# Optimization experiments

Measured on AMD Instinct MI355X. Metric: run time of the kernel, lower is better.

Reference implementation:

```python
import jax, jax.numpy as jnp
import numpy as np

# ---- static config (matches init_kwargs) ----
B, N, DIM = 1, 2048, 1024
H, KVH, D = 16, 8, 64
GQ = H // KVH                 # grouped queries per kv head
WS = 64                       # sliding window size (causal, exact)
CBS, STRIDE = 32, 16          # compress block size / sliding stride
SEL_BLK, NSEL, NMEM = 32, 4, 1
NCB = N // STRIDE             # num compressed blocks (128)
NFB = N // SEL_BLK            # num fine blocks (64)
NCPF = SEL_BLK // STRIDE      # compressed blocks per fine block (2)
HID = CBS * D                 # compress MLP hidden (expand factor 1.0)
SCALE = D ** -0.5
THETA = 10000.0
NEG = -jnp.finfo(jnp.float32).max


def setup_inputs():
    key = jax.random.key(0)
    ks = jax.random.split(key, 16)
    s = 0.02
    r = lambda i, shape: jax.random.normal(ks[i], shape, jnp.float32) * s
    return {
        "inp": jax.random.normal(ks[0], (B, N, DIM), jnp.float32),
        "norm_g": jnp.ones((DIM,), jnp.float32),
        "Wqkv": r(1, (DIM, (H + 2 * KVH) * D)),
        "mem_kv": r(2, (2, KVH, NMEM, D)),
        "k_pos": r(3, (KVH, CBS, D)),
        "v_pos": r(4, (KVH, CBS, D)),
        "kW1": r(5, (CBS * D, HID)), "kb1": jnp.zeros((HID,), jnp.float32),
        "kW2": r(6, (HID, D)), "kb2": jnp.zeros((D,), jnp.float32),
        "vW1": r(7, (CBS * D, HID)), "vb1": jnp.zeros((HID,), jnp.float32),
        "vW2": r(8, (HID, D)), "vb2": jnp.zeros((D,), jnp.float32),
        "combW": r(9, (DIM, 3 * H)),
        "combB": jnp.tile(jnp.array([-2.0, -2.0, 2.0], jnp.float32), H),
        "Wout": r(10, (H * D, DIM)),
    }


def _rope(t):
    # lucidrains rotary-embedding-torch: interleaved adjacent-pair rotation
    inv_freq = 1.0 / (THETA ** (jnp.arange(0, D, 2, dtype=jnp.float32) / D))
    ang = jnp.arange(N, dtype=jnp.float32)[:, None] * inv_freq        # [N, D/2]
    cos = jnp.repeat(jnp.cos(ang), 2, axis=-1)                        # [N, D]
    sin = jnp.repeat(jnp.sin(ang), 2, axis=-1)
    t2 = t.reshape(*t.shape[:-1], D // 2, 2)
    rot = jnp.stack([-t2[..., 1], t2[..., 0]], axis=-1).reshape(t.shape)
    return t * cos + rot * sin


def _forward(inp, norm_g, Wqkv, mem_kv, k_pos, v_pos,
             kW1, kb1, kW2, kb2, vW1, vb1, vW2, vb2,
             combW, combB, Wout):
    # RMSNorm
    x = inp * jax.lax.rsqrt(jnp.mean(inp * inp, -1, keepdims=True)
                            + jnp.finfo(inp.dtype).eps) * norm_g
    qkv = x @ Wqkv
    q, k, v = jnp.split(qkv, [H * D, H * D + KVH * D], axis=-1)
    q = q.reshape(B, N, H, D).transpose(0, 2, 1, 3)      # b h n d
    k = k.reshape(B, N, KVH, D).transpose(0, 2, 1, 3)    # b kvh n d
    v = v.reshape(B, N, KVH, D).transpose(0, 2, 1, 3)

    # ---- compressed branch (overlapping windows, left zero pad) ----
    overlap = CBS - STRIDE
    kp = jnp.pad(k, ((0, 0), (0, 0), (overlap, 0), (0, 0)))
    vp = jnp.pad(v, ((0, 0), (0, 0), (overlap, 0), (0, 0)))
    widx = jnp.arange(NCB)[:, None] * STRIDE + jnp.arange(CBS)[None, :]  # [NCB, CBS]
    kw = kp[:, :, widx] + k_pos[None, :, None]   # b kvh w cbs d
    vw = vp[:, :, widx] + v_pos[None, :, None]

    def cmlp(t, W1, b1, W2, b2):
        t = t.reshape(B, KVH, NCB, CBS * D)
        return jax.nn.relu(t @ W1 + b1) @ W2 + b2       # b kvh w d

    ck = cmlp(kw, kW1, kb1, kW2, kb2)
    cv = cmlp(vw, vW1, vb1, vW2, vb2)
    ck = jnp.concatenate([jnp.broadcast_to(mem_kv[0], (B, KVH, NMEM, D)), ck], 2)
    cv = jnp.concatenate([jnp.broadcast_to(mem_kv[1], (B, KVH, NMEM, D)), cv], 2)

    qg = q.reshape(B, KVH, GQ, N, D)
    csim = jnp.einsum('bhgid,bhjd->bhgij', qg, ck) * SCALE   # no mask (cmask=None)
    cattn = jax.nn.softmax(csim, -1)
    cout = jnp.einsum('bhgij,bhjd->bhgid', cattn, cv).reshape(B, H, N, D)

    # rotary AFTER compressed attention (as in source)
    rq, rk = _rope(q), _rope(k)

    # ---- importance scores -> top-k fine block selection ----
    imp = csim[..., NMEM:].mean(2)                          # b kvh n NCB (share grouped q)
    imp = imp.reshape(B, KVH, N, NFB, NCPF).mean(-1)        # mean-pool to fine blocks
    q_blk = jnp.arange(N) // SEL_BLK
    diag = q_blk[:, None] == jnp.arange(NFB)[None, :]
    imp = jnp.where(diag[None, None], NEG, imp)             # mask own (diagonal) block
    imp = jax.nn.softmax(jnp.pad(imp, ((0, 0),) * 3 + ((1, 0),),
                                 constant_values=-1000.0), -1)[..., 1:]
    sel_val, sel_idx = jax.lax.top_k(imp, NSEL)             # b kvh n NSEL

    # ---- fine (block-selected) attention ----
    own = jnp.broadcast_to(q_blk[None, None, :, None], (B, KVH, N, 1))
    sel_idx = jnp.concatenate([sel_idx, own], -1)           # append own block
    fmask = jnp.repeat((sel_val > 1e-10)[..., None], SEL_BLK, -1)  # b kvh n NSEL blk
    causal_row = jnp.tril(jnp.ones((SEL_BLK, SEL_BLK), bool))[jnp.arange(N) % SEL_BLK]
    causal = jnp.broadcast_to(causal_row[None, None, :, None, :],
                              (B, KVH, N, 1, SEL_BLK))
    fmask = jnp.concatenate([fmask, causal], 3).reshape(B, KVH, N, (NSEL + 1) * SEL_BLK)

    fk_blocks = rk.reshape(B, KVH, NFB, SEL_BLK, D)
    fv_blocks = v.reshape(B, KVH, NFB, SEL_BLK, D)
    gather = jax.vmap(jax.vmap(lambda blocks, idx: blocks[idx]))  # over b, kvh
    fk = gather(fk_blocks, sel_idx).reshape(B, KVH, N, (NSEL + 1) * SEL_BLK, D)
    fv = gather(fv_blocks, sel_idx).reshape(B, KVH, N, (NSEL + 1) * SEL_BLK, D)

    rqg = rq.reshape(B, KVH, GQ, N, D)
    fsim = jnp.einsum('bhgid,bhijd->bhgij', rqg, fk) * SCALE
    fsim = jnp.where(fmask[:, :, None], fsim, NEG / 10)
    fattn = jax.nn.softmax(fsim, -1)
    fout = jnp.einsum('bhgij,bhijd->bhgid', fattn, fv).reshape(B, H, N, D)

    # ---- sliding window (causal, exact window size WS) ----
    NW = N // WS
    kp2 = jnp.pad(rk, ((0, 0), (0, 0), (WS, 0), (0, 0)))
    vp2 = jnp.pad(v, ((0, 0), (0, 0), (WS, 0), (0, 0)))
    kidx = jnp.arange(NW)[:, None] * WS + jnp.arange(2 * WS)[None, :]
    kwin = kp2[:, :, kidx]                                  # b kvh nw 2ws d
    vwin = vp2[:, :, kidx]
    qwin = rqg.reshape(B, KVH, GQ, NW, WS, D)
    ssim = jnp.einsum('bhgwid,bhwjd->bhgwij', qwin, kwin) * SCALE
    i = jnp.arange(WS)[:, None]
    j = jnp.arange(2 * WS)[None, :]
    diff = i - (j - WS)
    local_ok = (diff >= 0) & (diff < WS)                    # [WS, 2WS]
    keypos = jnp.arange(NW)[:, None, None] * WS + (jnp.arange(2 * WS) - WS)[None, None, :]
    smask = local_ok[None] & (keypos >= 0)                  # [NW, WS, 2WS]
    ssim = jnp.where(smask[None, None, None], ssim, NEG)
    sattn = jax.nn.softmax(ssim, -1)
    sout = jnp.einsum('bhgwij,bhwjd->bhgwid', sattn, vwin).reshape(B, H, N, D)

    # ---- learned strategy combination (compressed, fine, sliding) ----
    gates = jax.nn.sigmoid(x @ combW + combB).reshape(B, N, H, 3).transpose(0, 2, 1, 3)
    out = gates[..., 0:1] * cout + gates[..., 1:2] * fout + gates[..., 2:3] * sout
    out = out.transpose(0, 2, 1, 3).reshape(B, N, H * D) @ Wout
    return out


def reference(inp, norm_g, Wqkv, mem_kv, k_pos, v_pos,
              kW1, kb1, kW2, kb2, vW1, vb1, vW2, vb2,
              combW, combB, Wout):
    return _forward(inp, norm_g, Wqkv, mem_kv, k_pos, v_pos,
                    kW1, kb1, kW2, kb2, vW1, vb1, vW2, vb2,
                    combW, combB, Wout)
```

## Files before the change

kernel.cpp:

```cpp
#include <hip/hip_runtime.h>
#include <hip/hip_bf16.h>

#define NTOK 2048
#define DIM 1024
#define NH 16
#define KVH 8
#define GQ 2
#define HD 64
#define WS 64
#define CBS 32
#define STRIDE 16
#define SEL_BLK 32
#define NSEL 4
#define NMEM 1
#define NCB 128
#define NFB 64
#define HIDN 2048
#define SCALE 0.125f
#define NEGF (-3.4028234663852886e38f)
#define NEG10F (-3.4028234663852886e37f)

typedef __attribute__((ext_vector_type(8))) short bf16x8;
typedef __attribute__((ext_vector_type(4))) float f32x4;

__device__ __forceinline__ float bflo(unsigned u) { return __uint_as_float(u << 16); }
__device__ __forceinline__ float bfhi(unsigned u) { return __uint_as_float(u & 0xffff0000u); }
__device__ __forceinline__ void dot8(const float4& qa, const float4& qb, uint4 a, float& s) {
    s += qa.x * bflo(a.x) + qa.y * bfhi(a.x) + qa.z * bflo(a.y) + qa.w * bfhi(a.y) +
         qb.x * bflo(a.z) + qb.y * bfhi(a.z) + qb.z * bflo(a.w) + qb.w * bfhi(a.w);
}

__device__ __forceinline__ void gload_lds16(const void* g, void* l) {
    __builtin_amdgcn_global_load_lds((const __attribute__((address_space(1))) unsigned*)g,
                                     (__attribute__((address_space(3))) unsigned*)l, 16, 0, 0);
}

__device__ __forceinline__ void rms_body(const float* __restrict__ inp,
                                         const float* __restrict__ g,
                                         float* __restrict__ x,
                                         __hip_bfloat16* __restrict__ xb, int n) {
    const float* row = inp + (size_t)n * DIM;
    float ss = 0.f;
    for (int c = threadIdx.x; c < DIM; c += 256) { float v = row[c]; ss += v * v; }
    __shared__ float red[4];
    for (int o = 32; o; o >>= 1) ss += __shfl_down(ss, o, 64);
    if ((threadIdx.x & 63) == 0) red[threadIdx.x >> 6] = ss;
    __syncthreads();
    if (threadIdx.x == 0) red[0] = red[0] + red[1] + red[2] + red[3];
    __syncthreads();
    float rs = 1.0f / sqrtf(red[0] / (float)DIM + 1.1920928955078125e-07f);
    float* xr = x + (size_t)n * DIM;
    __hip_bfloat16* xbr = xb + (size_t)n * DIM;
    for (int c = threadIdx.x; c < DIM; c += 256) {
        float v = row[c] * rs * g[c];
        xr[c] = v;
        xbr[c] = __float2bfloat16(v);
    }
}

__device__ __forceinline__ void transpose_body(const float* __restrict__ B,
                                               __hip_bfloat16* __restrict__ Bt,
                                               int K, int N, int bx, int by) {
    __shared__ float tile[32][33];
    int n0 = bx * 32, k0 = by * 32;
    int x = threadIdx.x & 31, y = threadIdx.x >> 5;
    for (int i = 0; i < 4; i++) {
        int k = k0 + y + 8 * i, n = n0 + x;
        tile[y + 8 * i][x] = (k < K && n < N) ? B[(size_t)k * N + n] : 0.f;
    }
    __syncthreads();
    for (int i = 0; i < 4; i++) {
        int n = n0 + y + 8 * i, k = k0 + x;
        if (n < N && k < K) Bt[(size_t)n * K + k] = __float2bfloat16(tile[x][y + 8 * i]);
    }
}

__global__ __launch_bounds__(256) void pre_kernel(
    const float* inp, const float* norm_g, float* x, __hip_bfloat16* xb,
    const float* Wqkv, __hip_bfloat16* Wqkvt,
    const float* kW1, __hip_bfloat16* kW1t,
    const float* vW1, __hip_bfloat16* vW1t,
    const float* Wout, __hip_bfloat16* Woutt,
    const float* combW, __hip_bfloat16* combWt,
    const float* kW2, __hip_bfloat16* kW2t,
    const float* vW2, __hip_bfloat16* vW2t,
    const float* combB, float* gatesb,
    const float* kb2, float* ckraw,
    const float* vb2, float* cvraw) {
    int b = blockIdx.x;
    if (b < 2048) { rms_body(inp, norm_g, x, xb, b); return; }
    b -= 2048;
    if (b < 2048) { transpose_body(Wqkv, Wqkvt, 1024, 2048, b % 64, b / 64); return; }
    b -= 2048;
    if (b < 4096) { transpose_body(kW1, kW1t, 2048, 2048, b % 64, b / 64); return; }
    b -= 4096;
    if (b < 4096) { transpose_body(vW1, vW1t, 2048, 2048, b % 64, b / 64); return; }
    b -= 4096;
    if (b < 1024) { transpose_body(Wout, Woutt, 1024, 1024, b % 32, b / 32); return; }
    b -= 1024;
    if (b < 64) { transpose_body(combW, combWt, 1024, 48, b % 2, b / 2); return; }
    b -= 64;
    if (b < 128) { transpose_body(kW2, kW2t, 2048, 64, b % 2, b / 2); return; }
    b -= 128;
    if (b < 128) { transpose_body(vW2, vW2t, 2048, 64, b % 2, b / 2); return; }
    b -= 128;
    if (b < 384) {
        int idx = b * 256 + threadIdx.x;
        if (idx < 2048 * 48) gatesb[idx] = combB[idx % 48];
        return;
    }
    b -= 384;
    {
        int idx = b * 256 + threadIdx.x;
        int tot = 1024 * 64;
        if (idx < tot) ckraw[idx] = kb2[idx % 64];
        else if (idx < 2 * tot) { idx -= tot; cvraw[idx] = vb2[idx % 64]; }
        return;
    }
}
#define PRE_BLOCKS (2048 + 2048 + 4096 + 4096 + 1024 + 64 + 128 + 128 + 384 + 512)

template <int ACT, int OUTBF16>
__device__ __forceinline__ void mfma_gemm_body(const __hip_bfloat16* __restrict__ A,
                                               const __hip_bfloat16* __restrict__ Bt,
                                               const float* __restrict__ bias,
                                               void* __restrict__ Cp,
                                               int M, int N, int K, int bx, int by) {
    __shared__ __align__(16) short As[128 * 32];
    __shared__ __align__(16) short Bs[128 * 32];
    int tid = threadIdx.x;
    int lane = tid & 63, wave = tid >> 6;
    int wm = (wave >> 1) * 64, wn = (wave & 1) * 64;
    int m0 = by * 128, n0 = bx * 128;
    f32x4 acc[4][4];
    for (int r = 0; r < 4; r++)
        for (int c = 0; c < 4; c++)
            acc[r][c] = (f32x4){0.f, 0.f, 0.f, 0.f};

    int r0 = tid >> 2, kc0 = (tid & 3) * 8;
    int r1 = r0 + 64;

    for (int k0 = 0; k0 < K; k0 += 32) {
        __syncthreads();
        gload_lds16(A + (size_t)(m0 + r0) * K + k0 + kc0, &As[r0 * 32 + kc0]);
        gload_lds16(A + (size_t)(m0 + r1) * K + k0 + kc0, &As[r1 * 32 + kc0]);
        gload_lds16(Bt + (size_t)(n0 + r0) * K + k0 + kc0, &Bs[r0 * 32 + kc0]);
        gload_lds16(Bt + (size_t)(n0 + r1) * K + k0 + kc0, &Bs[r1 * 32 + kc0]);
        __syncthreads();
        bf16x8 af[4], bfr[4];
#pragma unroll
        for (int r = 0; r < 4; r++)
            af[r] = *(const bf16x8*)&As[(wm + r * 16 + (lane & 15)) * 32 + (lane >> 4) * 8];
#pragma unroll
        for (int c = 0; c < 4; c++)
            bfr[c] = *(const bf16x8*)&Bs[(wn + c * 16 + (lane & 15)) * 32 + (lane >> 4) * 8];
#pragma unroll
        for (int r = 0; r < 4; r++)
#pragma unroll
            for (int c = 0; c < 4; c++)
                acc[r][c] = __builtin_amdgcn_mfma_f32_16x16x32_bf16(af[r], bfr[c], acc[r][c], 0, 0, 0);
    }
    for (int r = 0; r < 4; r++) {
        int grow = m0 + wm + r * 16 + (lane >> 4) * 4;
        for (int c = 0; c < 4; c++) {
            int gcol = n0 + wn + c * 16 + (lane & 15);
            float bv = bias ? bias[gcol] : 0.f;
#pragma unroll
            for (int v = 0; v < 4; v++) {
                float val = acc[r][c][v] + bv;
                if (ACT == 1) val = fmaxf(val, 0.f);
                if (OUTBF16)
                    ((__hip_bfloat16*)Cp)[(size_t)(grow + v) * N + gcol] = __float2bfloat16(val);
                else
                    ((float*)Cp)[(size_t)(grow + v) * N + gcol] = val;
            }
        }
    }
}

template <int ACT, int OUTBF16>
__global__ __launch_bounds__(256) void mfma_gemm(const __hip_bfloat16* __restrict__ A,
                                                 const __hip_bfloat16* __restrict__ Bt,
                                                 const float* __restrict__ bias,
                                                 void* __restrict__ Cp,
                                                 int M, int N, int K) {
    mfma_gemm_body<ACT, OUTBF16>(A, Bt, bias, Cp, M, N, K, blockIdx.x, blockIdx.y);
}

__global__ __launch_bounds__(256) void mfma_gemm_pair(const __hip_bfloat16* A0,
                                                      const __hip_bfloat16* A1,
                                                      const __hip_bfloat16* Bt0,
                                                      const __hip_bfloat16* Bt1,
                                                      const float* bias0, const float* bias1,
                                                      __hip_bfloat16* C0, __hip_bfloat16* C1,
                                                      int M, int N, int K) {
    if (blockIdx.z == 0)
        mfma_gemm_body<1, 1>(A0, Bt0, bias0, C0, M, N, K, blockIdx.x, blockIdx.y);
    else
        mfma_gemm_body<1, 1>(A1, Bt1, bias1, C1, M, N, K, blockIdx.x, blockIdx.y);
}

__device__ __forceinline__ void skgemm_body(const __hip_bfloat16* __restrict__ A,
                                            const __hip_bfloat16* __restrict__ Bt,
                                            float* __restrict__ C,
                                            int M, int Nout, int K, int by, int bz, int nz) {
    __shared__ __align__(16) short As2[128 * 32];
    __shared__ __align__(16) short Bs2[64 * 32];
    int tid = threadIdx.x;
    int lane = tid & 63, wave = tid >> 6;
    int m0 = by * 128;
    int wm = wave * 32;
    int kchunk = K / nz;
    int kbase = bz * kchunk;
    f32x4 acc[2][4];
    for (int r = 0; r < 2; r++)
        for (int c = 0; c < 4; c++) acc[r][c] = (f32x4){0.f, 0.f, 0.f, 0.f};

    int ra = tid >> 2, kc = (tid & 3) * 8;
    int rb = ra < Nout ? ra : Nout - 1;
    for (int k0 = kbase; k0 < kbase + kchunk; k0 += 32) {
        __syncthreads();
        gload_lds16(A + (size_t)(m0 + ra) * K + k0 + kc, &As2[ra * 32 + kc]);
        gload_lds16(A + (size_t)(m0 + ra + 64) * K + k0 + kc, &As2[(ra + 64) * 32 + kc]);
        gload_lds16(Bt + (size_t)rb * K + k0 + kc, &Bs2[ra * 32 + kc]);
        __syncthreads();
        bf16x8 af[2], bfr[4];
#pragma unroll
        for (int r = 0; r < 2; r++)
            af[r] = *(const bf16x8*)&As2[(wm + r * 16 + (lane & 15)) * 32 + (lane >> 4) * 8];
#pragma unroll
        for (int c = 0; c < 4; c++)
            bfr[c] = *(const bf16x8*)&Bs2[(c * 16 + (lane & 15)) * 32 + (lane >> 4) * 8];
#pragma unroll
        for (int r = 0; r < 2; r++)
#pragma unroll
            for (int c = 0; c < 4; c++)
                acc[r][c] = __builtin_amdgcn_mfma_f32_16x16x32_bf16(af[r], bfr[c], acc[r][c], 0, 0, 0);
    }
    for (int r = 0; r < 2; r++) {
        int grow = m0 + wm + r * 16 + (lane >> 4) * 4;
        for (int c = 0; c < 4; c++) {
            int gcol = c * 16 + (lane & 15);
            if (gcol >= Nout) continue;
#pragma unroll
            for (int v = 0; v < 4; v++)
                atomicAdd(&C[(size_t)(grow + v) * Nout + gcol], acc[r][c][v]);
        }
    }
}

__global__ __launch_bounds__(256) void qkv_gates_kernel(const __hip_bfloat16* xb,
                                                        const __hip_bfloat16* Wqkvt,
                                                        float* qkv,
                                                        const __hip_bfloat16* combWt,
                                                        float* gatesb) {
    int b = blockIdx.x;
    if (b < 256) {
        mfma_gemm_body<0, 0>(xb, Wqkvt, nullptr, qkv, 2048, 2048, 1024, b & 15, b >> 4);
    } else {
        int s = b - 256;
        skgemm_body(xb, combWt, gatesb, 2048, 48, 1024, s & 15, s >> 4, 4);
    }
}

__global__ __launch_bounds__(256) void skgemm_pair(const __hip_bfloat16* A0,
                                                   const __hip_bfloat16* A1,
                                                   const __hip_bfloat16* Bt0,
                                                   const __hip_bfloat16* Bt1,
                                                   float* C0, float* C1,
                                                   int M, int Nout, int K) {
    if (blockIdx.x == 0)
        skgemm_body(A0, Bt0, C0, M, Nout, K, blockIdx.y, blockIdx.z, gridDim.z);
    else
        skgemm_body(A1, Bt1, C1, M, Nout, K, blockIdx.y, blockIdx.z, gridDim.z);
}

__global__ __launch_bounds__(256) void winrope_kernel(const float* __restrict__ qkv,
                                                      const float* __restrict__ k_pos,
                                                      const float* __restrict__ v_pos,
                                                      __hip_bfloat16* __restrict__ kwflat,
                                                      __hip_bfloat16* __restrict__ vwflat,
                                                      float* __restrict__ rq,
                                                      __hip_bfloat16* __restrict__ rk,
                                                      __hip_bfloat16* __restrict__ vt) {
    int b = blockIdx.x;
    int t = threadIdx.x;
    if (b < 4096) {
        size_t total = (size_t)(KVH * NCB) * HIDN;
        for (size_t e = (size_t)b * 256 + t; e < total; e += (size_t)4096 * 256) {
            int r = (int)(e >> 11);
            int c = (int)(e & 2047);
            int j = c >> 6, d = c & 63;
            int h = r >> 7, i = r & 127;
            int p = i * STRIDE + j - (CBS - STRIDE);
            float kb = k_pos[((size_t)h * CBS + j) * HD + d];
            float vb = v_pos[((size_t)h * CBS + j) * HD + d];
            float kv = 0.f, vv = 0.f;
            if (p >= 0) {
                kv = qkv[(size_t)p * 2048 + 1024 + h * HD + d];
                vv = qkv[(size_t)p * 2048 + 1536 + h * HD + d];
            }
            kwflat[e] = __float2bfloat16(kv + kb);
            vwflat[e] = __float2bfloat16(vv + vb);
        }
        return;
    }
    int n = b - 4096;
    for (int idx = t; idx < NH * 32; idx += 256) {
        int h = idx >> 5, f = idx & 31;
        float inv = exp2f((float)f * -0.41524101186092f);
        float ang = (float)n * inv;
        float cc = cosf(ang), ssn = sinf(ang);
        float a = qkv[(size_t)n * 2048 + h * HD + 2 * f];
        float bq = qkv[(size_t)n * 2048 + h * HD + 2 * f + 1];
        float* o = rq + ((size_t)h * NTOK + n) * HD + 2 * f;
        o[0] = a * cc - bq * ssn;
        o[1] = bq * cc + a * ssn;
    }
    for (int idx = t; idx < KVH * 32; idx += 256) {
        int h = idx >> 5, f = idx & 31;
        float inv = exp2f((float)f * -0.41524101186092f);
        float ang = (float)n * inv;
        float cc = cosf(ang), ssn = sinf(ang);
        float a = qkv[(size_t)n * 2048 + 1024 + h * HD + 2 * f];
        float bq = qkv[(size_t)n * 2048 + 1024 + h * HD + 2 * f + 1];
        __hip_bfloat16* o = rk + ((size_t)h * NTOK + n) * HD + 2 * f;
        o[0] = __float2bfloat16(a * cc - bq * ssn);
        o[1] = __float2bfloat16(bq * cc + a * ssn);
    }
    for (int idx = t; idx < KVH * HD; idx += 256) {
        int h = idx >> 6, d = idx & 63;
        vt[((size_t)h * NTOK + n) * HD + d] =
            __float2bfloat16(qkv[(size_t)n * 2048 + 1536 + h * HD + d]);
    }
}

__global__ __launch_bounds__(256) void cattn2_kernel(const float* __restrict__ qkv,
                                                     const float* __restrict__ ckraw,
                                                     const float* __restrict__ cvraw,
                                                     const float* __restrict__ memkv,
                                                     float* __restrict__ cout,
                                                     int* __restrict__ selidx,
                                                     int* __restrict__ selmask) {
    int h = blockIdx.x >> 6;
    int i0 = (blockIdx.x & 63) * 32;
    int t = threadIdx.x;
    __shared__ float qs[64][68];
    __shared__ float sc[64][132];
    __shared__ float scratch[32 * 68];
    __shared__ float memk[64], memv[64];

    for (int idx = t; idx < 4096; idx += 256) {
        int row = idx >> 6, d = idx & 63;
        int g = row >> 5, qi = row & 31;
        qs[row][d] = qkv[(size_t)(i0 + qi) * 2048 + (h * 2 + g) * 64 + d];
    }
    if (t < 64) { memk[t] = memkv[h * 64 + t]; memv[t] = memkv[(8 + h) * 64 + t]; }
    __syncthreads();
    if (t < 64) {
        float s = 0.f;
        for (int d = 0; d < 64; d++) s += qs[t][d] * memk[d];
        sc[t][0] = s * SCALE;
    }
    int rg = t >> 3, kg = t & 7;
    for (int c = 0; c < 4; c++) {
        __syncthreads();
        for (int idx = t; idx < 2048; idx += 256) {
            int jj = idx >> 6, d = idx & 63;
            scratch[jj * 68 + d] = ckraw[((size_t)h * 128 + c * 32 + jj) * 64 + d];
        }
        __syncthreads();
        float a0[4] = {}, a1[4] = {};
        for (int d = 0; d < 64; d += 4) {
            float4 q0 = *(const float4*)&qs[rg * 2][d];
            float4 q1 = *(const float4*)&qs[rg * 2 + 1][d];
#pragma unroll
            for (int kk = 0; kk < 4; kk++) {
                float4 kv = *(const float4*)&scratch[(kg + kk * 8) * 68 + d];
                a0[kk] += q0.x * kv.x + q0.y * kv.y + q0.z * kv.z + q0.w * kv.w;
                a1[kk] += q1.x * kv.x + q1.y * kv.y + q1.z * kv.z + q1.w * kv.w;
            }
        }
#pragma unroll
        for (int kk = 0; kk < 4; kk++) {
            sc[rg * 2][1 + c * 32 + kg + kk * 8] = a0[kk] * SCALE;
            sc[rg * 2 + 1][1 + c * 32 + kg + kk * 8] = a1[kk] * SCALE;
        }
    }
    __syncthreads();
    for (int idx = t; idx < 2048; idx += 256) {
        int qi = idx >> 6, fb = idx & 63;
        float v = 0.25f * (sc[qi][1 + 2 * fb] + sc[qi][2 + 2 * fb] +
                           sc[32 + qi][1 + 2 * fb] + sc[32 + qi][2 + 2 * fb]);
        if (fb == ((i0 + qi) >> 5)) v = NEGF;
        scratch[qi * 66 + fb] = v;
    }
    __syncthreads();
    if (t < 32) {
        float* row = &scratch[t * 66];
        float m = -1000.f;
        for (int j = 0; j < 64; j++) m = fmaxf(m, row[j]);
        float den = __expf(-1000.f - m);
        for (int j = 0; j < 64; j++) den += __expf(row[j] - m);
        float invd = 1.f / den;
        unsigned long long taken = 0ull;
        int mk = 0;
        size_t base = ((size_t)h * NTOK + i0 + t) * 5;
        for (int p = 0; p < NSEL; p++) {
            float bv = NEGF;
            int bi = 0;
            for (int j = 0; j < 64; j++) {
                if (!((taken >> j) & 1ull) && row[j] > bv) { bv = row[j]; bi = j; }
            }
            taken |= 1ull << bi;
            selidx[base + p] = bi;
            if (__expf(bv - m) * invd > 1e-10f) mk |= 1 << p;
        }
        selidx[base + 4] = (i0 + t) >> 5;
        selmask[h * NTOK + i0 + t] = mk;
    } else if (t >= 64 && t < 128) {
        int r = t - 64;
        float m = NEGF;
        for (int j = 0; j < 129; j++) m = fmaxf(m, sc[r][j]);
        float den = 0.f;
        for (int j = 0; j < 129; j++) { float e = __expf(sc[r][j] - m); sc[r][j] = e; den += e; }
        float inv = 1.f / den;
        for (int j = 0; j < 129; j++) sc[r][j] *= inv;
    }
    __syncthreads();
    int dg = t & 7;
    float o0[8], o1[8];
    {
        float p0 = sc[rg * 2][0], p1 = sc[rg * 2 + 1][0];
#pragma unroll
        for (int dd = 0; dd < 8; dd++) {
            float v = memv[dg + dd * 8];
            o0[dd] = p0 * v;
            o1[dd] = p1 * v;
        }
    }
    for (int c = 0; c < 4; c++) {
        __syncthreads();
        for (int idx = t; idx < 2048; idx += 256) {
            int jj = idx >> 6, d = idx & 63;
            scratch[jj * 68 + d] = cvraw[((size_t)h * 128 + c * 32 + jj) * 64 + d];
        }
        __syncthreads();
        for (int jj = 0; jj < 32; jj++) {
            float p0 = sc[rg * 2][1 + c * 32 + jj];
            float p1 = sc[rg * 2 + 1][1 + c * 32 + jj];
#pragma unroll
            for (int dd = 0; dd < 8; dd++) {
                float v = scratch[jj * 68 + dg + dd * 8];
                o0[dd] += p0 * v;
                o1[dd] += p1 * v;
            }
        }
    }
    {
        int row = rg * 2;
        int g = row >> 5, qi = row & 31;
        int g2 = (row + 1) >> 5, qi2 = (row + 1) & 31;
#pragma unroll
        for (int dd = 0; dd < 8; dd++) {
            cout[(((size_t)(h * 2 + g)) * NTOK + i0 + qi) * 64 + dd * 8 + dg] = o0[dd];
            cout[(((size_t)(h * 2 + g2)) * NTOK + i0 + qi2) * 64 + dd * 8 + dg] = o1[dd];
        }
    }
}

#define SLIDE_BLKS 1024
#define SROWS 79
#define SPAD 72
#define SLIDE_LDS (SROWS * SPAD * 2 * 2 + 4 * 128 * 4)
__global__ __launch_bounds__(256) void attn_fused4_kernel(const float* __restrict__ rq,
                                                          const __hip_bfloat16* __restrict__ rk,
                                                          const __hip_bfloat16* __restrict__ vt,
                                                          const int* __restrict__ selidx,
                                                          const int* __restrict__ selmask,
                                                          float* __restrict__ fout,
                                                          float* __restrict__ sout) {
    int tid = threadIdx.x;
    int ws = tid >> 6, lane = tid & 63;
    __shared__ __align__(16) char smem[SLIDE_LDS];

    int kq = lane >> 2, c = lane & 3;
    int kv8 = lane >> 3, c8 = lane & 7;

    if (blockIdx.x < SLIDE_BLKS) {
        int h = blockIdx.x & 7;
        int q0 = (int)(blockIdx.x >> 3) * 16;
        short* ks = (short*)smem;
        short* vs = ks + SROWS * SPAD;
        float* ps = (float*)(smem + SROWS * SPAD * 2 * 2);
        int basek = q0 - 63;
        for (int idx = tid; idx < SROWS * 8; idx += 256) {
            int row = idx >> 3, ch = (idx & 7) * 8;
            int kpos = basek + row;
            uint4 kv = (uint4){0u, 0u, 0u, 0u}, vv = (uint4){0u, 0u, 0u, 0u};
            if (kpos >= 0) {
                kv = *(const uint4*)(rk + ((size_t)h * NTOK + kpos) * 64 + ch);
                vv = *(const uint4*)(vt + ((size_t)h * NTOK + kpos) * 64 + ch);
            }
            *(uint4*)&ks[row * SPAD + ch] = kv;
            *(uint4*)&vs[row * SPAD + ch] = vv;
        }
        __syncthreads();
        float* p0 = ps + ws * 128;
        float* p1 = p0 + 64;
#pragma unroll 1
        for (int tq = 0; tq < 4; tq++) {
            int ibase = ws * 4 + tq;
            int i = q0 + ibase;
            const float* q0p = rq + ((size_t)(h * 2 + 0) * NTOK + i) * 64 + c * 16;
            const float* q1p = rq + ((size_t)(h * 2 + 1) * NTOK + i) * 64 + c * 16;
            float4 qa[4], qb[4];
#pragma unroll
            for (int u = 0; u < 4; u++) {
                qa[u] = *(const float4*)(q0p + u * 4);
                qb[u] = *(const float4*)(q1p + u * 4);
            }
#pragma unroll
            for (int kt = 0; kt < 4; kt++) {
                int key = kt * 16 + kq;
                const short* kr = &ks[(ibase + key) * SPAD + c * 16];
                float s0 = 0.f, s1 = 0.f;
                uint4 a = *(const uint4*)(kr);
                uint4 b = *(const uint4*)(kr + 8);
                dot8(qa[0], qa[1], a, s0); dot8(qa[2], qa[3], b, s0);
                dot8(qb[0], qb[1], a, s1); dot8(qb[2], qb[3], b, s1);
                s0 += __shfl_xor(s0, 1); s0 += __shfl_xor(s0, 2);
                s1 += __shfl_xor(s1, 1); s1 += __shfl_xor(s1, 2);
                int kpos = i - 63 + key;
                if (c == 0) {
                    p0[key] = (kpos >= 0) ? s0 * SCALE : NEG10F;
                    p1[key] = (kpos >= 0) ? s1 * SCALE : NEG10F;
                }
            }
            {
                float a0 = p0[lane], a1 = p1[lane];
                float m0 = a0, m1 = a1;
#pragma unroll
                for (int o = 1; o < 64; o <<= 1) {
                    m0 = fmaxf(m0, __shfl_xor(m0, o));
                    m1 = fmaxf(m1, __shfl_xor(m1, o));
                }
                float e0 = __expf(a0 - m0), e1 = __expf(a1 - m1);
                float d0 = e0, d1 = e1;
#pragma unroll
                for (int o = 1; o < 64; o <<= 1) {
                    d0 += __shfl_xor(d0, o);
                    d1 += __shfl_xor(d1, o);
                }
                p0[lane] = e0 / d0;
                p1[lane] = e1 / d1;
            }
            float o0[8] = {}, o1[8] = {};
#pragma unroll
            for (int pass = 0; pass < 8; pass++) {
                int j = pass * 8 + kv8;
                uint4 v = *(const uint4*)&vs[(ibase + j) * SPAD + c8 * 8];
                float pa = p0[j], pb = p1[j];
                float e0 = bflo(v.x), e1 = bfhi(v.x), e2 = bflo(v.y), e3 = bfhi(v.y);
                float e4 = bflo(v.z), e5 = bfhi(v.z), e6 = bflo(v.w), e7 = bfhi(v.w);
                o0[0] = fmaf(pa, e0, o0[0]); o0[1] = fmaf(pa, e1, o0[1]);
                o0[2] = fmaf(pa, e2, o0[2]); o0[3] = fmaf(pa, e3, o0[3]);
                o0[4] = fmaf(pa, e4, o0[4]); o0[5] = fmaf(pa, e5, o0[5]);
                o0[6] = fmaf(pa, e6, o0[6]); o0[7] = fmaf(pa, e7, o0[7]);
                o1[0] = fmaf(pb, e0, o1[0]); o1[1] = fmaf(pb, e1, o1[1]);
                o1[2] = fmaf(pb, e2, o1[2]); o1[3] = fmaf(pb, e3, o1[3]);
                o1[4] = fmaf(pb, e4, o1[4]); o1[5] = fmaf(pb, e5, o1[5]);
                o1[6] = fmaf(pb, e6, o1[6]); o1[7] = fmaf(pb, e7, o1[7]);
            }
#pragma unroll
            for (int o = 8; o <= 32; o <<= 1)
#pragma unroll
                for (int d = 0; d < 8; d++) {
                    o0[d] += __shfl_xor(o0[d], o);
                    o1[d] += __shfl_xor(o1[d], o);
                }
            if (kv8 == 0) {
                float* s0p = sout + ((size_t)(h * 2 + 0) * NTOK + i) * 64 + c8 * 8;
                float* s1p = sout + ((size_t)(h * 2 + 1) * NTOK + i) * 64 + c8 * 8;
                *(float4*)(s0p) = (float4){o0[0], o0[1], o0[2], o0[3]};
                *(float4*)(s0p + 4) = (float4){o0[4], o0[5], o0[6], o0[7]};
                *(float4*)(s1p) = (float4){o1[0], o1[1], o1[2], o1[3]};
                *(float4*)(s1p + 4) = (float4){o1[4], o1[5], o1[6], o1[7]};
            }
        }
    } else {
        int bb = blockIdx.x - SLIDE_BLKS;
        int h = bb & 7;
        int i = (bb >> 3) * 4 + ws;
        float* pbuf = (float*)smem;
        float* pf0 = pbuf + ws * 320;
        float* pf1 = pf0 + 160;

        size_t sbase = ((size_t)h * NTOK + i) * 5;
        int selr[5];
#pragma unroll
        for (int s = 0; s < 5; s++) selr[s] = selidx[sbase + s];
        int mk = selmask[h * NTOK + i];

        const float* q0p = rq + ((size_t)(h * 2 + 0) * NTOK + i) * 64 + c * 16;
        const float* q1p = rq + ((size_t)(h * 2 + 1) * NTOK + i) * 64 + c * 16;
        float4 q0[4], q1[4];
#pragma unroll
        for (int u = 0; u < 4; u++) {
            q0[u] = *(const float4*)(q0p + u * 4);
            q1[u] = *(const float4*)(q1p + u * 4);
        }
        int iq = i & 31;

#pragma unroll
        for (int kt = 0; kt < 10; kt++) {
            int slot = kt >> 1;
            int blk = selr[slot];
            int key = kt * 16 + kq;
            int jj = key & 31;
            int kpos = blk * 32 + jj;
            bool valid = (slot < 4) ? (((mk >> slot) & 1) != 0) : (jj <= iq);
            const __hip_bfloat16* kr = rk + ((size_t)h * NTOK + kpos) * 64 + c * 16;
            float s0 = 0.f, s1 = 0.f;
            uint4 a = *(const uint4*)(kr);
            uint4 b = *(const uint4*)(kr + 8);
            dot8(q0[0], q0[1], a, s0); dot8(q0[2], q0[3], b, s0);
            dot8(q1[0], q1[1], a, s1); dot8(q1[2], q1[3], b, s1);
            s0 += __shfl_xor(s0, 1); s0 += __shfl_xor(s0, 2);
            s1 += __shfl_xor(s1, 1); s1 += __shfl_xor(s1, 2);
            if (c == 0) {
                pf0[key] = valid ? s0 * SCALE : NEG10F;
                pf1[key] = valid ? s1 * SCALE : NEG10F;
            }
        }
        {
            float a0 = pf0[lane], b0 = pf0[lane + 64];
            float c0 = (lane < 32) ? pf0[lane + 128] : NEG10F;
            float a1 = pf1[lane], b1 = pf1[lane + 64];
            float c1 = (lane < 32) ? pf1[lane + 128] : NEG10F;
            float m0 = fmaxf(fmaxf(a0, b0), c0);
            float m1 = fmaxf(fmaxf(a1, b1), c1);
#pragma unroll
            for (int o = 1; o < 64; o <<= 1) {
                m0 = fmaxf(m0, __shfl_xor(m0, o));
                m1 = fmaxf(m1, __shfl_xor(m1, o));
            }
            float ea0 = __expf(a0 - m0), eb0 = __expf(b0 - m0), ec0 = (lane < 32) ? __expf(c0 - m0) : 0.f;
            float ea1 = __expf(a1 - m1), eb1 = __expf(b1 - m1), ec1 = (lane < 32) ? __expf(c1 - m1) : 0.f;
            float d0 = ea0 + eb0 + ec0;
            float d1 = ea1 + eb1 + ec1;
#pragma unroll
            for (int o = 1; o < 64; o <<= 1) {
                d0 += __shfl_xor(d0, o);
                d1 += __shfl_xor(d1, o);
            }
            float inv0 = 1.f / d0, inv1 = 1.f / d1;
            pf0[lane] = ea0 * inv0; pf0[lane + 64] = eb0 * inv0;
            pf1[lane] = ea1 * inv1; pf1[lane + 64] = eb1 * inv1;
            if (lane < 32) { pf0[lane + 128] = ec0 * inv0; pf1[lane + 128] = ec1 * inv1; }
        }
        float o0[8] = {}, o1[8] = {};
#pragma unroll
        for (int slot = 0; slot < 5; slot++) {
            const __hip_bfloat16* vbase = vt + ((size_t)h * NTOK + selr[slot] * 32) * 64;
#pragma unroll
            for (int pass = 0; pass < 4; pass++) {
                int j = pass * 8 + kv8;
                uint4 v = *(const uint4*)(vbase + j * 64 + c8 * 8);
                float pa = pf0[slot * 32 + j], pb = pf1[slot * 32 + j];
                float e0 = bflo(v.x), e1 = bfhi(v.x), e2 = bflo(v.y), e3 = bfhi(v.y);
                float e4 = bflo(v.z), e5 = bfhi(v.z), e6 = bflo(v.w), e7 = bfhi(v.w);
                o0[0] = fmaf(pa, e0, o0[0]); o0[1] = fmaf(pa, e1, o0[1]);
                o0[2] = fmaf(pa, e2, o0[2]); o0[3] = fmaf(pa, e3, o0[3]);
                o0[4] = fmaf(pa, e4, o0[4]); o0[5] = fmaf(pa, e5, o0[5]);
                o0[6] = fmaf(pa, e6, o0[6]); o0[7] = fmaf(pa, e7, o0[7]);
                o1[0] = fmaf(pb, e0, o1[0]); o1[1] = fmaf(pb, e1, o1[1]);
                o1[2] = fmaf(pb, e2, o1[2]); o1[3] = fmaf(pb, e3, o1[3]);
                o1[4] = fmaf(pb, e4, o1[4]); o1[5] = fmaf(pb, e5, o1[5]);
                o1[6] = fmaf(pb, e6, o1[6]); o1[7] = fmaf(pb, e7, o1[7]);
            }
        }
#pragma unroll
        for (int o = 8; o <= 32; o <<= 1)
#pragma unroll
            for (int d = 0; d < 8; d++) {
                o0[d] += __shfl_xor(o0[d], o);
                o1[d] += __shfl_xor(o1[d], o);
            }
        if (kv8 == 0) {
            float* f0 = fout + ((size_t)(h * 2 + 0) * NTOK + i) * 64 + c8 * 8;
            float* f1 = fout + ((size_t)(h * 2 + 1) * NTOK + i) * 64 + c8 * 8;
            *(float4*)(f0) = (float4){o0[0], o0[1], o0[2], o0[3]};
            *(float4*)(f0 + 4) = (float4){o0[4], o0[5], o0[6], o0[7]};
            *(float4*)(f1) = (float4){o1[0], o1[1], o1[2], o1[3]};
            *(float4*)(f1 + 4) = (float4){o1[4], o1[5], o1[6], o1[7]};
        }
    }
}

__global__ __launch_bounds__(256) void combine_kernel(const float* __restrict__ gateslin,
                                                      const float* __restrict__ cout,
                                                      const float* __restrict__ fout,
                                                      const float* __restrict__ sout,
                                                      __hip_bfloat16* __restrict__ att) {
    int n = blockIdx.x;
    for (int c = threadIdx.x; c < NH * HD; c += 256) {
        int hd = c >> 6, d = c & 63;
        float g0 = 1.f / (1.f + expf(-gateslin[(size_t)n * (NH * 3) + hd * 3 + 0]));
        float g1 = 1.f / (1.f + expf(-gateslin[(size_t)n * (NH * 3) + hd * 3 + 1]));
        float g2 = 1.f / (1.f + expf(-gateslin[(size_t)n * (NH * 3) + hd * 3 + 2]));
        size_t o = ((size_t)hd * NTOK + n) * HD + d;
        att[(size_t)n * (NH * HD) + c] =
            __float2bfloat16(g0 * cout[o] + g1 * fout[o] + g2 * sout[o]);
    }
}

extern "C" void kernel_launch(void* const* d_in, const int* in_sizes, int n_in,
                              void* d_out, int out_size, void* d_ws, size_t ws_size,
                              hipStream_t stream) {
    const float* inp    = (const float*)d_in[0];
    const float* norm_g = (const float*)d_in[1];
    const float* Wqkv   = (const float*)d_in[2];
    const float* mem_kv = (const float*)d_in[3];
    const float* k_pos  = (const float*)d_in[4];
    const float* v_pos  = (const float*)d_in[5];
    const float* kW1    = (const float*)d_in[6];
    const float* kb1    = (const float*)d_in[7];
    const float* kW2    = (const float*)d_in[8];
    const float* kb2    = (const float*)d_in[9];
    const float* vW1    = (const float*)d_in[10];
    const float* vb1    = (const float*)d_in[11];
    const float* vW2    = (const float*)d_in[12];
    const float* vb2    = (const float*)d_in[13];
    const float* combW  = (const float*)d_in[14];
    const float* combB  = (const float*)d_in[15];
    const float* Wout   = (const float*)d_in[16];
    float* out = (float*)d_out;

    char* base = (char*)d_ws;
    size_t off = 0;
    auto alloc = [&](size_t bytes) {
        void* p = base + off;
        off += (bytes + 255) & ~(size_t)255;
        return p;
    };
    float* x            = (float*)alloc((size_t)NTOK * DIM * 4);
    __hip_bfloat16* xb  = (__hip_bfloat16*)alloc((size_t)NTOK * DIM * 2);
    float* qkv          = (float*)alloc((size_t)NTOK * 2048 * 4);
    __hip_bfloat16* Wqkvt = (__hip_bfloat16*)alloc((size_t)2048 * 1024 * 2);
    __hip_bfloat16* kW1t  = (__hip_bfloat16*)alloc((size_t)2048 * 2048 * 2);
    __hip_bfloat16* vW1t  = (__hip_bfloat16*)alloc((size_t)2048 * 2048 * 2);
    __hip_bfloat16* Woutt = (__hip_bfloat16*)alloc((size_t)1024 * 1024 * 2);
    __hip_bfloat16* combWt = (__hip_bfloat16*)alloc((size_t)48 * 1024 * 2);
    __hip_bfloat16* kW2t  = (__hip_bfloat16*)alloc((size_t)64 * 2048 * 2);
    __hip_bfloat16* vW2t  = (__hip_bfloat16*)alloc((size_t)64 * 2048 * 2);
    __hip_bfloat16* kwflat = (__hip_bfloat16*)alloc((size_t)KVH * NCB * HIDN * 2);
    __hip_bfloat16* vwflat = (__hip_bfloat16*)alloc((size_t)KVH * NCB * HIDN * 2);
    __hip_bfloat16* hidkb = (__hip_bfloat16*)alloc((size_t)KVH * NCB * HIDN * 2);
    __hip_bfloat16* hidvb = (__hip_bfloat16*)alloc((size_t)KVH * NCB * HIDN * 2);
    float* ckraw        = (float*)alloc((size_t)KVH * NCB * HD * 4);
    float* cvraw        = (float*)alloc((size_t)KVH * NCB * HD * 4);
    float* rq           = (float*)alloc((size_t)NH * NTOK * HD * 4);
    __hip_bfloat16* rk  = (__hip_bfloat16*)alloc((size_t)KVH * NTOK * HD * 2);
    __hip_bfloat16* vt  = (__hip_bfloat16*)alloc((size_t)KVH * NTOK * HD * 2);
    float* coutb        = (float*)alloc((size_t)NH * NTOK * HD * 4);
    float* foutb        = (float*)alloc((size_t)NH * NTOK * HD * 4);
    float* soutb        = (float*)alloc((size_t)NH * NTOK * HD * 4);
    float* gatesb       = (float*)alloc((size_t)NTOK * NH * 3 * 4);
    __hip_bfloat16* attb = (__hip_bfloat16*)alloc((size_t)NTOK * DIM * 2);
    int* selidx         = (int*)alloc((size_t)KVH * NTOK * 5 * 4);
    int* selmask        = (int*)alloc((size_t)KVH * NTOK * 4);
    (void)ws_size; (void)in_sizes; (void)n_in; (void)out_size;

    pre_kernel<<<PRE_BLOCKS, 256, 0, stream>>>(inp, norm_g, x, xb,
                                               Wqkv, Wqkvt, kW1, kW1t, vW1, vW1t,
                                               Wout, Woutt, combW, combWt,
                                               kW2, kW2t, vW2, vW2t,
                                               combB, gatesb, kb2, ckraw, vb2, cvraw);
    qkv_gates_kernel<<<320, 256, 0, stream>>>(xb, Wqkvt, qkv, combWt, gatesb);
    winrope_kernel<<<4096 + 2048, 256, 0, stream>>>(qkv, k_pos, v_pos, kwflat, vwflat,
                                                    rq, rk, vt);
    mfma_gemm_pair<<<dim3(16, 8, 2), 256, 0, stream>>>(kwflat, vwflat, kW1t, vW1t,
                                                       kb1, vb1, hidkb, hidvb,
                                                       1024, 2048, 2048);
    skgemm_pair<<<dim3(2, 8, 8), 256, 0, stream>>>(hidkb, hidvb, kW2t, vW2t,
                                                   ckraw, cvraw, 1024, 64, 2048);
    cattn2_kernel<<<KVH * (NTOK / 32), 256, 0, stream>>>(qkv, ckraw, cvraw, mem_kv,
                                                         coutb, selidx, selmask);
    attn_fused4_kernel<<<SLIDE_BLKS + 4096, 256, 0, stream>>>(rq, rk, vt, selidx, selmask,
                                                              foutb, soutb);
    combine_kernel<<<NTOK, 256, 0, stream>>>(gatesb, coutb, foutb, soutb, attb);
    mfma_gemm<0, 0><<<dim3(8, 16), 256, 0, stream>>>(attb, Woutt, nullptr, out, 2048, 1024, 1024);
}
```

Before: 371.4 us.

## Store rotated Q/K in fp16 with packed half2 dot products; shrink GEMM tiles to 128x64

Rotated queries and keys are now stored as fp16 instead of fp32/bf16, and the attention score dot products use packed __hfma2 accumulation in half precision before converting to float. This halves Q memory traffic and cuts ALU work in the sliding and fine attention paths, at the cost of fp16 accumulation error over 8-term partial sums. Separately, all MFMA GEMMs move from 128x128 tiles to 128x64 tiles, doubling the block count to improve CU occupancy on the modest-sized GEMMs, though each block gets less operand reuse.

```diff
diff --git a/kernel.cpp b/kernel.cpp
--- a/kernel.cpp
+++ b/kernel.cpp
@@ -1,5 +1,6 @@
 #include <hip/hip_runtime.h>
 #include <hip/hip_bf16.h>
+#include <hip/hip_fp16.h>
 
 #define NTOK 2048
 #define DIM 1024
@@ -25,9 +26,20 @@
 
 __device__ __forceinline__ float bflo(unsigned u) { return __uint_as_float(u << 16); }
 __device__ __forceinline__ float bfhi(unsigned u) { return __uint_as_float(u & 0xffff0000u); }
-__device__ __forceinline__ void dot8(const float4& qa, const float4& qb, uint4 a, float& s) {
-    s += qa.x * bflo(a.x) + qa.y * bfhi(a.x) + qa.z * bflo(a.y) + qa.w * bfhi(a.y) +
-         qb.x * bflo(a.z) + qb.y * bfhi(a.z) + qb.z * bflo(a.w) + qb.w * bfhi(a.w);
+
+union HU { uint4 v[2]; __half2 h[8]; };
+
+__device__ __forceinline__ void dot16h(const HU& k, const HU& qa, const HU& qb,
+                                       float& s0, float& s1) {
+    __half2 a0 = __float2half2_rn(0.f), a1 = __float2half2_rn(0.f);
+#pragma unroll
+    for (int j = 0; j < 8; j++) {
+        a0 = __hfma2(k.h[j], qa.h[j], a0);
+        a1 = __hfma2(k.h[j], qb.h[j], a1);
+    }
+    float2 f0 = __half22float2(a0), f1 = __half22float2(a1);
+    s0 += f0.x + f0.y;
+    s1 += f1.x + f1.y;
 }
 
 __device__ __forceinline__ void gload_lds16(const void* g, void* l) {
@@ -121,49 +133,45 @@
 #define PRE_BLOCKS (2048 + 2048 + 4096 + 4096 + 1024 + 64 + 128 + 128 + 384 + 512)
 
 template <int ACT, int OUTBF16>
-__device__ __forceinline__ void mfma_gemm_body(const __hip_bfloat16* __restrict__ A,
-                                               const __hip_bfloat16* __restrict__ Bt,
-                                               const float* __restrict__ bias,
-                                               void* __restrict__ Cp,
-                                               int M, int N, int K, int bx, int by) {
-    __shared__ __align__(16) short As[128 * 32];
-    __shared__ __align__(16) short Bs[128 * 32];
+__device__ __forceinline__ void gemm64_body(const __hip_bfloat16* __restrict__ A,
+                                            const __hip_bfloat16* __restrict__ Bt,
+                                            const float* __restrict__ bias,
+                                            void* __restrict__ Cp,
+                                            int M, int N, int K, int bx, int by) {
+    __shared__ __align__(16) short As2[128 * 32];
+    __shared__ __align__(16) short Bs2[64 * 32];
     int tid = threadIdx.x;
     int lane = tid & 63, wave = tid >> 6;
-    int wm = (wave >> 1) * 64, wn = (wave & 1) * 64;
-    int m0 = by * 128, n0 = bx * 128;
-    f32x4 acc[4][4];
-    for (int r = 0; r < 4; r++)
+    int m0 = by * 128, n0 = bx * 64;
+    int wm = wave * 32;
+    f32x4 acc[2][4];
+    for (int r = 0; r < 2; r++)
+        for (int c = 0; c < 4; c++) acc[r][c] = (f32x4){0.f, 0.f, 0.f, 0.f};
+
+    int ra = tid >> 2, kc = (tid & 3) * 8;
+    for (int k0 = 0; k0 < K; k0 += 32) {
+        __syncthreads();
+        gload_lds16(A + (size_t)(m0 + ra) * K + k0 + kc, &As2[ra * 32 + kc]);
+        gload_lds16(A + (size_t)(m0 + ra + 64) * K + k0 + kc, &As2[(ra + 64) * 32 + kc]);
+        gload_lds16(Bt + (size_t)(n0 + ra) * K + k0 + kc, &Bs2[ra * 32 + kc]);
+        __syncthreads();
+        bf16x8 af[2], bfr[4];
+#pragma unroll
+        for (int r = 0; r < 2; r++)
+            af[r] = *(const bf16x8*)&As2[(wm + r * 16 + (lane & 15)) * 32 + (lane >> 4) * 8];
+#pragma unroll
         for (int c = 0; c < 4; c++)
-            acc[r][c] = (f32x4){0.f, 0.f, 0.f, 0.f};
-
-    int r0 = tid >> 2, kc0 = (tid & 3) * 8;
-    int r1 = r0 + 64;
-
-    for (int k0 = 0; k0 < K; k0 += 32) {
-        __syncthreads();
-        gload_lds16(A + (size_t)(m0 + r0) * K + k0 + kc0, &As[r0 * 32 + kc0]);
-        gload_lds16(A + (size_t)(m0 + r1) * K + k0 + kc0, &As[r1 * 32 + kc0]);
-        gload_lds16(Bt + (size_t)(n0 + r0) * K + k0 + kc0, &Bs[r0 * 32 + kc0]);
-        gload_lds16(Bt + (size_t)(n0 + r1) * K + k0 + kc0, &Bs[r1 * 32 + kc0]);
-        __syncthreads();
-        bf16x8 af[4], bfr[4];
-#pragma unroll
-        for (int r = 0; r < 4; r++)
-            af[r] = *(const bf16x8*)&As[(wm + r * 16 + (lane & 15)) * 32 + (lane >> 4) * 8];
-#pragma unroll
-        for (int c = 0; c < 4; c++)
-            bfr[c] = *(const bf16x8*)&Bs[(wn + c * 16 + (lane & 15)) * 32 + (lane >> 4) * 8];
-#pragma unroll
-        for (int r = 0; r < 4; r++)
+            bfr[c] = *(const bf16x8*)&Bs2[(c * 16 + (lane & 15)) * 32 + (lane >> 4) * 8];
+#pragma unroll
+        for (int r = 0; r < 2; r++)
 #pragma unroll
             for (int c = 0; c < 4; c++)
                 acc[r][c] = __builtin_amdgcn_mfma_f32_16x16x32_bf16(af[r], bfr[c], acc[r][c], 0, 0, 0);
     }
-    for (int r = 0; r < 4; r++) {
+    for (int r = 0; r < 2; r++) {
         int grow = m0 + wm + r * 16 + (lane >> 4) * 4;
         for (int c = 0; c < 4; c++) {
-            int gcol = n0 + wn + c * 16 + (lane & 15);
+            int gcol = n0 + c * 16 + (lane & 15);
             float bv = bias ? bias[gcol] : 0.f;
 #pragma unroll
             for (int v = 0; v < 4; v++) {
@@ -179,25 +187,25 @@
 }
 
 template <int ACT, int OUTBF16>
-__global__ __launch_bounds__(256) void mfma_gemm(const __hip_bfloat16* __restrict__ A,
-                                                 const __hip_bfloat16* __restrict__ Bt,
-                                                 const float* __restrict__ bias,
-                                                 void* __restrict__ Cp,
-                                                 int M, int N, int K) {
-    mfma_gemm_body<ACT, OUTBF16>(A, Bt, bias, Cp, M, N, K, blockIdx.x, blockIdx.y);
-}
-
-__global__ __launch_bounds__(256) void mfma_gemm_pair(const __hip_bfloat16* A0,
-                                                      const __hip_bfloat16* A1,
-                                                      const __hip_bfloat16* Bt0,
-                                                      const __hip_bfloat16* Bt1,
-                                                      const float* bias0, const float* bias1,
-                                                      __hip_bfloat16* C0, __hip_bfloat16* C1,
-                                                      int M, int N, int K) {
+__global__ __launch_bounds__(256) void gemm64(const __hip_bfloat16* __restrict__ A,
+                                              const __hip_bfloat16* __restrict__ Bt,
+                                              const float* __restrict__ bias,
+                                              void* __restrict__ Cp,
+                                              int M, int N, int K) {
+    gemm64_body<ACT, OUTBF16>(A, Bt, bias, Cp, M, N, K, blockIdx.x, blockIdx.y);
+}
+
+__global__ __launch_bounds__(256) void gemm64_pair(const __hip_bfloat16* A0,
+                                                   const __hip_bfloat16* A1,
+                                                   const __hip_bfloat16* Bt0,
+                                                   const __hip_bfloat16* Bt1,
+                                                   const float* bias0, const float* bias1,
+                                                   __hip_bfloat16* C0, __hip_bfloat16* C1,
+                                                   int M, int N, int K) {
     if (blockIdx.z == 0)
-        mfma_gemm_body<1, 1>(A0, Bt0, bias0, C0, M, N, K, blockIdx.x, blockIdx.y);
+        gemm64_body<1, 1>(A0, Bt0, bias0, C0, M, N, K, blockIdx.x, blockIdx.y);
     else
-        mfma_gemm_body<1, 1>(A1, Bt1, bias1, C1, M, N, K, blockIdx.x, blockIdx.y);
+        gemm64_body<1, 1>(A1, Bt1, bias1, C1, M, N, K, blockIdx.x, blockIdx.y);
 }
 
 __device__ __forceinline__ void skgemm_body(const __hip_bfloat16* __restrict__ A,
@@ -255,10 +263,10 @@
                                                         const __hip_bfloat16* combWt,
                                                         float* gatesb) {
     int b = blockIdx.x;
-    if (b < 256) {
-        mfma_gemm_body<0, 0>(xb, Wqkvt, nullptr, qkv, 2048, 2048, 1024, b & 15, b >> 4);
+    if (b < 512) {
+        gemm64_body<0, 0>(xb, Wqkvt, nullptr, qkv, 2048, 2048, 1024, b & 31, b >> 5);
     } else {
-        int s = b - 256;
+        int s = b - 512;
         skgemm_body(xb, combWt, gatesb, 2048, 48, 1024, s & 15, s >> 4, 4);
     }
 }
@@ -280,8 +288,8 @@
                                                       const float* __restrict__ v_pos,
                                                       __hip_bfloat16* __restrict__ kwflat,
                                                       __hip_bfloat16* __restrict__ vwflat,
-                                                      float* __restrict__ rq,
-                                                      __hip_bfloat16* __restrict__ rk,
+                                                      __half* __restrict__ rqh,
+                                                      __half* __restrict__ rkh,
                                                       __hip_bfloat16* __restrict__ vt) {
     int b = blockIdx.x;
     int t = threadIdx.x;
@@ -313,9 +321,9 @@
         float cc = cosf(ang), ssn = sinf(ang);
         float a = qkv[(size_t)n * 2048 + h * HD + 2 * f];
         float bq = qkv[(size_t)n * 2048 + h * HD + 2 * f + 1];
-        float* o = rq + ((size_t)h * NTOK + n) * HD + 2 * f;
-        o[0] = a * cc - bq * ssn;
-        o[1] = bq * cc + a * ssn;
+        __half* o = rqh + ((size_t)h * NTOK + n) * HD + 2 * f;
+        o[0] = __float2half(a * cc - bq * ssn);
+        o[1] = __float2half(bq * cc + a * ssn);
     }
     for (int idx = t; idx < KVH * 32; idx += 256) {
         int h = idx >> 5, f = idx & 31;
@@ -324,9 +332,9 @@
         float cc = cosf(ang), ssn = sinf(ang);
         float a = qkv[(size_t)n * 2048 + 1024 + h * HD + 2 * f];
         float bq = qkv[(size_t)n * 2048 + 1024 + h * HD + 2 * f + 1];
-        __hip_bfloat16* o = rk + ((size_t)h * NTOK + n) * HD + 2 * f;
-        o[0] = __float2bfloat16(a * cc - bq * ssn);
-        o[1] = __float2bfloat16(bq * cc + a * ssn);
+        __half* o = rkh + ((size_t)h * NTOK + n) * HD + 2 * f;
+        o[0] = __float2half(a * cc - bq * ssn);
+        o[1] = __float2half(bq * cc + a * ssn);
     }
     for (int idx = t; idx < KVH * HD; idx += 256) {
         int h = idx >> 6, d = idx & 63;
@@ -473,8 +481,8 @@
 #define SROWS 79
 #define SPAD 72
 #define SLIDE_LDS (SROWS * SPAD * 2 * 2 + 4 * 128 * 4)
-__global__ __launch_bounds__(256) void attn_fused4_kernel(const float* __restrict__ rq,
-                                                          const __hip_bfloat16* __restrict__ rk,
+__global__ __launch_bounds__(256) void attn_fused5_kernel(const __half* __restrict__ rqh,
+                                                          const __half* __restrict__ rkh,
                                                           const __hip_bfloat16* __restrict__ vt,
                                                           const int* __restrict__ selidx,
                                                           const int* __restrict__ selmask,
@@ -499,7 +507,7 @@
             int kpos = basek + row;
             uint4 kv = (uint4){0u, 0u, 0u, 0u}, vv = (uint4){0u, 0u, 0u, 0u};
             if (kpos >= 0) {
-                kv = *(const uint4*)(rk + ((size_t)h * NTOK + kpos) * 64 + ch);
+                kv = *(const uint4*)(rkh + ((size_t)h * NTOK + kpos) * 64 + ch);
                 vv = *(const uint4*)(vt + ((size_t)h * NTOK + kpos) * 64 + ch);
             }
             *(uint4*)&ks[row * SPAD + ch] = kv;
@@ -512,23 +520,20 @@
         for (int tq = 0; tq < 4; tq++) {
             int ibase = ws * 4 + tq;
             int i = q0 + ibase;
-            const float* q0p = rq + ((size_t)(h * 2 + 0) * NTOK + i) * 64 + c * 16;
-            const float* q1p = rq + ((size_t)(h * 2 + 1) * NTOK + i) * 64 + c * 16;
-            float4 qa[4], qb[4];
-#pragma unroll
-            for (int u = 0; u < 4; u++) {
-                qa[u] = *(const float4*)(q0p + u * 4);
-                qb[u] = *(const float4*)(q1p + u * 4);
-            }
+            const __half* q0p = rqh + ((size_t)(h * 2 + 0) * NTOK + i) * 64 + c * 16;
+            const __half* q1p = rqh + ((size_t)(h * 2 + 1) * NTOK + i) * 64 + c * 16;
+            HU qa, qb;
+            qa.v[0] = *(const uint4*)(q0p); qa.v[1] = *(const uint4*)(q0p + 8);
+            qb.v[0] = *(const uint4*)(q1p); qb.v[1] = *(const uint4*)(q1p + 8);
 #pragma unroll
             for (int kt = 0; kt < 4; kt++) {
                 int key = kt * 16 + kq;
                 const short* kr = &ks[(ibase + key) * SPAD + c * 16];
+                HU kk_;
+                kk_.v[0] = *(const uint4*)(kr);
+                kk_.v[1] = *(const uint4*)(kr + 8);
                 float s0 = 0.f, s1 = 0.f;
-                uint4 a = *(const uint4*)(kr);
-                uint4 b = *(const uint4*)(kr + 8);
-                dot8(qa[0], qa[1], a, s0); dot8(qa[2], qa[3], b, s0);
-                dot8(qb[0], qb[1], a, s1); dot8(qb[2], qb[3], b, s1);
+                dot16h(kk_, qa, qb, s0, s1);
                 s0 += __shfl_xor(s0, 1); s0 += __shfl_xor(s0, 2);
                 s1 += __shfl_xor(s1, 1); s1 += __shfl_xor(s1, 2);
                 int kpos = i - 63 + key;
@@ -602,14 +607,11 @@
         for (int s = 0; s < 5; s++) selr[s] = selidx[sbase + s];
         int mk = selmask[h * NTOK + i];
 
-        const float* q0p = rq + ((size_t)(h * 2 + 0) * NTOK + i) * 64 + c * 16;
-        const float* q1p = rq + ((size_t)(h * 2 + 1) * NTOK + i) * 64 + c * 16;
-        float4 q0[4], q1[4];
-#pragma unroll
-        for (int u = 0; u < 4; u++) {
-            q0[u] = *(const float4*)(q0p + u * 4);
-            q1[u] = *(const float4*)(q1p + u * 4);
-        }
+        const __half* q0p = rqh + ((size_t)(h * 2 + 0) * NTOK + i) * 64 + c * 16;
+        const __half* q1p = rqh + ((size_t)(h * 2 + 1) * NTOK + i) * 64 + c * 16;
+        HU qa, qb;
+        qa.v[0] = *(const uint4*)(q0p); qa.v[1] = *(const uint4*)(q0p + 8);
+        qb.v[0] = *(const uint4*)(q1p); qb.v[1] = *(const uint4*)(q1p + 8);
         int iq = i & 31;
 
 #pragma unroll
@@ -620,12 +622,12 @@
             int jj = key & 31;
             int kpos = blk * 32 + jj;
             bool valid = (slot < 4) ? (((mk >> slot) & 1) != 0) : (jj <= iq);
-            const __hip_bfloat16* kr = rk + ((size_t)h * NTOK + kpos) * 64 + c * 16;
+            const __half* kr = rkh + ((size_t)h * NTOK + kpos) * 64 + c * 16;
+            HU kk_;
+            kk_.v[0] = *(const uint4*)(kr);
+            kk_.v[1] = *(const uint4*)(kr + 8);
             float s0 = 0.f, s1 = 0.f;
-            uint4 a = *(const uint4*)(kr);
-            uint4 b = *(const uint4*)(kr + 8);
-            dot8(q0[0], q0[1], a, s0); dot8(q0[2], q0[3], b, s0);
-            dot8(q1[0], q1[1], a, s1); dot8(q1[2], q1[3], b, s1);
+            dot16h(kk_, qa, qb, s0, s1);
             s0 += __shfl_xor(s0, 1); s0 += __shfl_xor(s0, 2);
             s1 += __shfl_xor(s1, 1); s1 += __shfl_xor(s1, 2);
             if (c == 0) {
@@ -760,8 +762,8 @@
     __hip_bfloat16* hidvb = (__hip_bfloat16*)alloc((size_t)KVH * NCB * HIDN * 2);
     float* ckraw        = (float*)alloc((size_t)KVH * NCB * HD * 4);
     float* cvraw        = (float*)alloc((size_t)KVH * NCB * HD * 4);
-    float* rq           = (float*)alloc((size_t)NH * NTOK * HD * 4);
-    __hip_bfloat16* rk  = (__hip_bfloat16*)alloc((size_t)KVH * NTOK * HD * 2);
+    __half* rqh         = (__half*)alloc((size_t)NH * NTOK * HD * 2);
+    __half* rkh         = (__half*)alloc((size_t)KVH * NTOK * HD * 2);
     __hip_bfloat16* vt  = (__hip_bfloat16*)alloc((size_t)KVH * NTOK * HD * 2);
     float* coutb        = (float*)alloc((size_t)NH * NTOK * HD * 4);
     float* foutb        = (float*)alloc((size_t)NH * NTOK * HD * 4);
@@ -777,18 +779,18 @@
                                                Wout, Woutt, combW, combWt,
                                                kW2, kW2t, vW2, vW2t,
                                                combB, gatesb, kb2, ckraw, vb2, cvraw);
-    qkv_gates_kernel<<<320, 256, 0, stream>>>(xb, Wqkvt, qkv, combWt, gatesb);
+    qkv_gates_kernel<<<576, 256, 0, stream>>>(xb, Wqkvt, qkv, combWt, gatesb);
     winrope_kernel<<<4096 + 2048, 256, 0, stream>>>(qkv, k_pos, v_pos, kwflat, vwflat,
-                                                    rq, rk, vt);
-    mfma_gemm_pair<<<dim3(16, 8, 2), 256, 0, stream>>>(kwflat, vwflat, kW1t, vW1t,
-                                                       kb1, vb1, hidkb, hidvb,
-                                                       1024, 2048, 2048);
+                                                    rqh, rkh, vt);
+    gemm64_pair<<<dim3(32, 8, 2), 256, 0, stream>>>(kwflat, vwflat, kW1t, vW1t,
+                                                    kb1, vb1, hidkb, hidvb,
+                                                    1024, 2048, 2048);
     skgemm_pair<<<dim3(2, 8, 8), 256, 0, stream>>>(hidkb, hidvb, kW2t, vW2t,
                                                    ckraw, cvraw, 1024, 64, 2048);
     cattn2_kernel<<<KVH * (NTOK / 32), 256, 0, stream>>>(qkv, ckraw, cvraw, mem_kv,
                                                          coutb, selidx, selmask);
-    attn_fused4_kernel<<<SLIDE_BLKS + 4096, 256, 0, stream>>>(rq, rk, vt, selidx, selmask,
+    attn_fused5_kernel<<<SLIDE_BLKS + 4096, 256, 0, stream>>>(rqh, rkh, vt, selidx, selmask,
                                                               foutb, soutb);
     combine_kernel<<<NTOK, 256, 0, stream>>>(gatesb, coutb, foutb, soutb, attb);
-    mfma_gemm<0, 0><<<dim3(8, 16), 256, 0, stream>>>(attb, Woutt, nullptr, out, 2048, 1024, 1024);
-}
+    gemm64<0, 0><<<dim3(16, 16), 256, 0, stream>>>(attb, Woutt, nullptr, out, 2048, 1024, 1024);
+}
```

Result: faster. 360.1 us (-3.0%).
